# Kernel tuning notes

Hardware: AMD Instinct MI355X
Metric: run time of the kernel (lower is better)

Reference implementation:

```python
import jax, jax.numpy as jnp
import numpy as np

B, N = 32, 512
IN, HID, HEADS, OUT = 128, 32, 4, 128
NEG_SLOPE = 0.2


def _ln(x, g, b, eps=1e-5):
    mu = x.mean(-1, keepdims=True)
    var = ((x - mu) ** 2).mean(-1, keepdims=True)
    return (x - mu) * jax.lax.rsqrt(var + eps) * g + b


def _gat(x, adj_mask, W, a_src, a_dst, average):
    # x: [B,N,F], adj_mask: [B,1,N,N] bool, W: [F,H,D], a_*: [H,D]
    h = jnp.einsum('bnf,fhd->bnhd', x, W)                      # [B,N,H,D]
    e_src = jnp.einsum('bnhd,hd->bhn', h, a_src)               # [B,H,N]
    e_dst = jnp.einsum('bnhd,hd->bhn', h, a_dst)
    e = jax.nn.leaky_relu(e_src[:, :, :, None] + e_dst[:, :, None, :], NEG_SLOPE)  # [B,H,N,N]
    e = jnp.where(adj_mask, e, jnp.asarray(-1e9, e.dtype))
    att = jax.nn.softmax(e, axis=-1)                           # masked softmax over neighbors
    out = jnp.einsum('bhnm,bmhd->bnhd', att, h)                # aggregate neighbor features
    if average:
        return out.mean(axis=2)                                # [B,N,D]
    return out.reshape(out.shape[0], out.shape[1], -1)         # concat heads [B,N,H*D]


def setup_inputs() -> dict:
    key = jax.random.key(0)
    ks = jax.random.split(key, 16)
    def nrm(k, shape, scale=0.05):
        return jax.random.normal(k, shape, dtype=jnp.float32) * scale
    return {
        'x': jax.random.normal(ks[0], (B, N, IN), dtype=jnp.float32),
        'graph': jax.random.randint(ks[1], (B, N, N), 0, 2, dtype=jnp.int32),
        'W0': nrm(ks[2], (IN, HEADS, HID)),
        'a_src0': nrm(ks[3], (HEADS, HID)),
        'a_dst0': nrm(ks[4], (HEADS, HID)),
        'W1': nrm(ks[5], (HEADS * HID, 1, OUT)),
        'a_src1': nrm(ks[6], (1, OUT)),
        'a_dst1': nrm(ks[7], (1, OUT)),
        'ln1_g': jnp.ones((IN + OUT,), jnp.float32), 'ln1_b': jnp.zeros((IN + OUT,), jnp.float32),
        'lin_W': nrm(ks[8], (IN + OUT, OUT)), 'lin_b': jnp.zeros((OUT,), jnp.float32),
        'me_W0': nrm(ks[9], (OUT, OUT)), 'me_b0': jnp.zeros((OUT,), jnp.float32),
        'me_W1': nrm(ks[10], (OUT, OUT)), 'me_b1': jnp.zeros((OUT,), jnp.float32),
        'ln2_g': jnp.ones((OUT,), jnp.float32), 'ln2_b': jnp.zeros((OUT,), jnp.float32),
        'oh_W': nrm(ks[11], (OUT, OUT)), 'oh_b': jnp.zeros((OUT,), jnp.float32),
        'ln3_g': jnp.ones((OUT,), jnp.float32), 'ln3_b': jnp.zeros((OUT,), jnp.float32),
    }


def reference(x, graph, W0, a_src0, a_dst0, W1, a_src1, a_dst1,
              ln1_g, ln1_b, lin_W, lin_b, me_W0, me_b0, me_W1, me_b1,
              ln2_g, ln2_b, oh_W, oh_b, ln3_g, ln3_b):
    eye = jnp.eye(N, dtype=bool)
    adj_mask = ((graph > 0) | eye)[:, None, :, :]              # self-loops, [B,1,N,N]
    m = _gat(x, adj_mask, W0, a_src0, a_dst0, average=False)   # [B,N,HEADS*HID]
    m = jax.nn.elu(m)
    m = _gat(m, adj_mask, W1, a_src1, a_dst1, average=True)    # [B,N,OUT]
    m = _ln(jnp.concatenate([x, m], axis=-1), ln1_g, ln1_b)    # ln1
    m = m @ lin_W + lin_b                                      # linear
    enc = jax.nn.gelu(m @ me_W0 + me_b0, approximate=False) @ me_W1 + me_b1
    out = _ln(m + enc, ln2_g, ln2_b)                           # ln2(residual)
    out = jax.nn.gelu(out @ oh_W + oh_b, approximate=False)
    out = _ln(out, ln3_g, ln3_b)                               # LN inside output_head
    return out
```

## Files before the change

### kernel.cpp

```cpp
#include <hip/hip_runtime.h>
#include <cmath>


typedef unsigned short ushort_t;
typedef __attribute__((ext_vector_type(8))) short short8;
typedef __attribute__((ext_vector_type(4))) float f32x4;

__device__ __forceinline__ float gelu_f(float v) {
    return 0.5f * v * (1.0f + erff(v * 0.70710678118654752f));
}
__device__ __forceinline__ ushort_t f2bf(float x) {
    union { float f; unsigned u; } v; v.f = x;
    return (ushort_t)((v.u + 0x7FFFu + ((v.u >> 16) & 1u)) >> 16);
}
__device__ __forceinline__ ushort_t f2bf_t(float x) {
    union { float f; unsigned u; } v; v.f = x;
    return (ushort_t)(v.u >> 16);
}

__global__ __launch_bounds__(256) void prep_wt(const float* __restrict__ lin_W,
        const float* __restrict__ me_W0, const float* __restrict__ me_W1,
        const float* __restrict__ oh_W, const float* __restrict__ W0,
        const float* __restrict__ W1, ushort_t* __restrict__ WT) {
    int i = blockIdx.x * 256 + threadIdx.x;
    if (i < 32768)       { int c = i >> 8, k = i & 255;                   WT[i] = f2bf(lin_W[k * 128 + c]); }
    else if (i < 49152)  { int j = i - 32768;  int c = j >> 7, k = j & 127; WT[i] = f2bf(me_W0[k * 128 + c]); }
    else if (i < 65536)  { int j = i - 49152;  int c = j >> 7, k = j & 127; WT[i] = f2bf(me_W1[k * 128 + c]); }
    else if (i < 81920)  { int j = i - 65536;  int c = j >> 7, k = j & 127; WT[i] = f2bf(oh_W[k * 128 + c]); }
    else if (i < 98304)  { int j = i - 81920;  int c = j >> 7, k = j & 127; WT[i] = f2bf(W0[k * 128 + c]); }
    else if (i < 114688) { int j = i - 98304;  int c = j >> 7, k = j & 127; WT[i] = f2bf(W1[k * 128 + c]); }
}

template<int MODE>
__global__ __launch_bounds__(256) void gemm_mfma(const float* __restrict__ X,
        const ushort_t* __restrict__ WTr, ushort_t* __restrict__ Ht,
        const float* __restrict__ a_s, const float* __restrict__ a_d,
        float* __restrict__ es, float* __restrict__ ed) {
    __shared__ __align__(16) ushort_t abuf[16 * 128];
    __shared__ __align__(16) ushort_t tb[128 * 24];
    __shared__ float2 ered[8 * 16];
    const int tid = threadIdx.x;
    const int row0 = blockIdx.x * 16;
    const int b = row0 >> 9, m0 = row0 & 511;
    const int w = tid >> 6, lane = tid & 63;
    const int quad = lane >> 4, lid = lane & 15;
    {
        int r = tid >> 4, g = tid & 15;
        const float4* src = (const float4*)(X + (row0 + r) * 128 + g * 8);
        float4 a = src[0], bb = src[1];
        short8 p;
        p[0] = (short)f2bf(a.x);  p[1] = (short)f2bf(a.y);
        p[2] = (short)f2bf(a.z);  p[3] = (short)f2bf(a.w);
        p[4] = (short)f2bf(bb.x); p[5] = (short)f2bf(bb.y);
        p[6] = (short)f2bf(bb.z); p[7] = (short)f2bf(bb.w);
        *(short8*)&abuf[r * 128 + ((g ^ (r & 7)) * 8)] = p;
    }
    __syncthreads();
    short8 af[4];
#pragma unroll
    for (int kc = 0; kc < 4; kc++)
        af[kc] = *(const short8*)&abuf[lid * 128 + (((kc * 4 + quad) ^ (lid & 7)) * 8)];
    f32x4 C[2];
#pragma unroll
    for (int i = 0; i < 2; i++) {
        int ct = w + 4 * i;
        const ushort_t* bp = WTr + (ct * 16 + lid) * 128 + quad * 8;
        C[i] = (f32x4){0.f, 0.f, 0.f, 0.f};
#pragma unroll
        for (int kc = 0; kc < 4; kc++) {
            short8 bf = *(const short8*)&bp[kc * 32];
            C[i] = __builtin_amdgcn_mfma_f32_16x16x32_bf16(af[kc], bf, C[i], 0, 0, 0);
        }
    }
#pragma unroll
    for (int i = 0; i < 2; i++) {
        int ct = w + 4 * i, col = ct * 16 + lid;
        float as_c = a_s[col], ad_c = a_d[col];
        float s0[4], d0[4];
#pragma unroll
        for (int r = 0; r < 4; r++) { s0[r] = C[i][r] * as_c; d0[r] = C[i][r] * ad_c; }
#pragma unroll
        for (int st = 1; st <= 8; st <<= 1)
#pragma unroll
            for (int r = 0; r < 4; r++) {
                s0[r] += __shfl_xor(s0[r], st);
                d0[r] += __shfl_xor(d0[r], st);
            }
        if (lid == 0) {
#pragma unroll
            for (int r = 0; r < 4; r++)
                ered[ct * 16 + quad * 4 + r] = make_float2(s0[r], d0[r]);
        }
    }
#pragma unroll
    for (int i = 0; i < 2; i++) {
        int c = (w + 4 * i) * 16 + lid;
#pragma unroll
        for (int r = 0; r < 4; r++)
            tb[c * 24 + quad * 4 + r] = f2bf(C[i][r]);
    }
    __syncthreads();
    if (MODE == 0) {
        if (tid < 64) {
            int row = tid & 15, h = tid >> 4;
            float2 pa = ered[(2 * h) * 16 + row], pb = ered[(2 * h + 1) * 16 + row];
            es[(b * 4 + h) * 512 + m0 + row] = pa.x + pb.x;
            ed[(b * 4 + h) * 512 + m0 + row] = pa.y + pb.y;
        }
    } else {
        if (tid < 16) {
            float S = 0.f, D = 0.f;
#pragma unroll
            for (int ct = 0; ct < 8; ct++) { float2 p = ered[ct * 16 + tid]; S += p.x; D += p.y; }
            es[b * 512 + m0 + tid] = S;
            ed[b * 512 + m0 + tid] = D;
        }
    }
    {
        int c = tid >> 1, half = tid & 1;
        *(short8*)&Ht[b * 65536 + c * 512 + m0 + half * 8] = *(const short8*)&tb[c * 24 + half * 8];
    }
}

__global__ __launch_bounds__(256) void gat0_mfma(const ushort_t* __restrict__ Ht,
        const float* __restrict__ es0, const float* __restrict__ ed0,
        const int* __restrict__ graph, float* __restrict__ O) {
    __shared__ __align__(16) ushort_t hsb[128 * 64];
    __shared__ __align__(16) ushort_t ps[64 * 64];
    __shared__ float eds[2048];
    __shared__ float ess[64];
    const int tid = threadIdx.x;
    const int b = blockIdx.y, n0 = blockIdx.x * 16;
    const int lane = tid & 63, wv = tid >> 6;
    const int quad = lane >> 4, lid = lane & 15;
    const int pn = tid >> 4, pg = (tid >> 1) & 7, ph = tid & 1;
    for (int i = tid; i < 2048; i += 256) eds[i] = ed0[b * 2048 + i];
    if (tid < 64) ess[tid] = es0[b * 2048 + (tid >> 4) * 512 + n0 + (tid & 15)];
    const short8 onesf = {0x3F80, 0x3F80, 0x3F80, 0x3F80, 0x3F80, 0x3F80, 0x3F80, 0x3F80};
    f32x4 acc[2], dsf;
    acc[0] = (f32x4){0.f, 0.f, 0.f, 0.f};
    acc[1] = (f32x4){0.f, 0.f, 0.f, 0.f};
    dsf = (f32x4){0.f, 0.f, 0.f, 0.f};
    for (int mc = 0; mc < 512; mc += 64) {
        __syncthreads();
        {
            const ushort_t* src = Ht + b * 65536 + mc;
            for (int u = tid; u < 1024; u += 256) {
                int c = u >> 3, g = u & 7;
                *(short8*)&hsb[c * 64 + ((g ^ (c & 7)) * 8)] = *(const short8*)&src[c * 512 + g * 8];
            }
        }
        {
            int ng = n0 + pn, mbase = mc + pg * 8;
            const int* grow = graph + (b * 512 + ng) * 512 + mbase;
            int4 ga = *(const int4*)grow;
            int4 gb = *(const int4*)(grow + 4);
            int gv[8] = {ga.x, ga.y, ga.z, ga.w, gb.x, gb.y, gb.z, gb.w};
            bool keep[8];
#pragma unroll
            for (int j = 0; j < 8; j++)
                keep[j] = (gv[j] > 0) | ((mbase + j) == ng);
#pragma unroll
            for (int hi = 0; hi < 2; hi++) {
                int hh = ph * 2 + hi;
                float es_v = ess[hh * 16 + pn];
                float4 e0v = *(const float4*)&eds[hh * 512 + mbase];
                float4 e1v = *(const float4*)&eds[hh * 512 + mbase + 4];
                float ev[8] = {e0v.x, e0v.y, e0v.z, e0v.w, e1v.x, e1v.y, e1v.z, e1v.w};
                short8 pk;
#pragma unroll
                for (int j = 0; j < 8; j++) {
                    float e = es_v + ev[j];
                    e = fmaxf(e, 0.2f * e);
                    e = keep[j] ? e : -1e30f;
                    pk[j] = (short)f2bf_t(__expf(e));
                }
                int prow = hh * 16 + pn;
                *(short8*)&ps[prow * 64 + ((pg ^ (prow & 7)) * 8)] = pk;
            }
        }
        __syncthreads();
#pragma unroll
        for (int kc = 0; kc < 2; kc++) {
            const int gsw = ((kc * 4 + quad) ^ (lid & 7)) * 8;
            short8 a = *(const short8*)&ps[(wv * 16 + lid) * 64 + gsw];
            short8 b0f = *(const short8*)&hsb[(wv * 32 + lid) * 64 + gsw];
            short8 b1f = *(const short8*)&hsb[(wv * 32 + 16 + lid) * 64 + gsw];
            acc[0] = __builtin_amdgcn_mfma_f32_16x16x32_bf16(a, b0f, acc[0], 0, 0, 0);
            acc[1] = __builtin_amdgcn_mfma_f32_16x16x32_bf16(a, b1f, acc[1], 0, 0, 0);
            dsf = __builtin_amdgcn_mfma_f32_16x16x32_bf16(a, onesf, dsf, 0, 0, 0);
        }
    }
#pragma unroll
    for (int reg = 0; reg < 4; reg++) {
        float inv = 1.0f / dsf[reg];
        int row = b * 512 + n0 + quad * 4 + reg;
#pragma unroll
        for (int ch = 0; ch < 2; ch++) {
            float v = acc[ch][reg] * inv;
            v = v > 0.f ? v : expm1f(v);
            O[row * 128 + wv * 32 + ch * 16 + lid] = v;
        }
    }
}

__global__ __launch_bounds__(256) void gat1_mfma(const ushort_t* __restrict__ Ht,
        const float* __restrict__ es1, const float* __restrict__ ed1,
        const int* __restrict__ graph, float* __restrict__ O) {
    __shared__ __align__(16) ushort_t hsb[128 * 64];
    __shared__ __align__(16) ushort_t ps[16 * 64];
    __shared__ float eds[512];
    __shared__ float ess[16];
    const int tid = threadIdx.x;
    const int b = blockIdx.y, n0 = blockIdx.x * 16;
    const int lane = tid & 63, wv = tid >> 6;
    const int quad = lane >> 4, lid = lane & 15;
    for (int i = tid; i < 512; i += 256) eds[i] = ed1[b * 512 + i];
    if (tid < 16) ess[tid] = es1[b * 512 + n0 + tid];
    const short8 onesf = {0x3F80, 0x3F80, 0x3F80, 0x3F80, 0x3F80, 0x3F80, 0x3F80, 0x3F80};
    f32x4 acc[2], dsf;
    acc[0] = (f32x4){0.f, 0.f, 0.f, 0.f};
    acc[1] = (f32x4){0.f, 0.f, 0.f, 0.f};
    dsf = (f32x4){0.f, 0.f, 0.f, 0.f};
    for (int mc = 0; mc < 512; mc += 64) {
        __syncthreads();
        {
            const ushort_t* src = Ht + b * 65536 + mc;
            for (int u = tid; u < 1024; u += 256) {
                int c = u >> 3, g = u & 7;
                *(short8*)&hsb[c * 64 + ((g ^ (c & 7)) * 8)] = *(const short8*)&src[c * 512 + g * 8];
            }
        }
        if (tid < 128) {
            int pn = tid >> 3, pg = tid & 7;
            int ng = n0 + pn, mbase = mc + pg * 8;
            const int* grow = graph + (b * 512 + ng) * 512 + mbase;
            int4 ga = *(const int4*)grow;
            int4 gb = *(const int4*)(grow + 4);
            int gv[8] = {ga.x, ga.y, ga.z, ga.w, gb.x, gb.y, gb.z, gb.w};
            float4 e0v = *(const float4*)&eds[mbase & 511];
            float4 e1v = *(const float4*)&eds[(mbase & 511) + 4];
            float ev[8] = {e0v.x, e0v.y, e0v.z, e0v.w, e1v.x, e1v.y, e1v.z, e1v.w};
            float es_v = ess[pn];
            short8 pk;
#pragma unroll
            for (int j = 0; j < 8; j++) {
                float e = es_v + ev[j];
                e = fmaxf(e, 0.2f * e);
                e = ((gv[j] > 0) | ((mbase + j) == ng)) ? e : -1e30f;
                pk[j] = (short)f2bf_t(__expf(e));
            }
            *(short8*)&ps[pn * 64 + ((pg ^ (pn & 7)) * 8)] = pk;
        }
        __syncthreads();
#pragma unroll
        for (int kc = 0; kc < 2; kc++) {
            const int gsw = ((kc * 4 + quad) ^ (lid & 7)) * 8;
            short8 a = *(const short8*)&ps[lid * 64 + gsw];
            short8 b0f = *(const short8*)&hsb[(wv * 32 + lid) * 64 + gsw];
            short8 b1f = *(const short8*)&hsb[(wv * 32 + 16 + lid) * 64 + gsw];
            acc[0] = __builtin_amdgcn_mfma_f32_16x16x32_bf16(a, b0f, acc[0], 0, 0, 0);
            acc[1] = __builtin_amdgcn_mfma_f32_16x16x32_bf16(a, b1f, acc[1], 0, 0, 0);
            dsf = __builtin_amdgcn_mfma_f32_16x16x32_bf16(a, onesf, dsf, 0, 0, 0);
        }
    }
#pragma unroll
    for (int reg = 0; reg < 4; reg++) {
        float inv = 1.0f / dsf[reg];
        int row = b * 512 + n0 + quad * 4 + reg;
#pragma unroll
        for (int ch = 0; ch < 2; ch++)
            O[row * 128 + wv * 32 + ch * 16 + lid] = acc[ch][reg] * inv;
    }
}

__global__ __launch_bounds__(256) void head_fused(const float* __restrict__ x,
        const float* __restrict__ G, const float* __restrict__ g1, const float* __restrict__ b1,
        const ushort_t* __restrict__ linT, const float* __restrict__ LB,
        const ushort_t* __restrict__ meT0, const float* __restrict__ B0,
        const ushort_t* __restrict__ meT1, const float* __restrict__ B1,
        const float* __restrict__ g2, const float* __restrict__ b2,
        const ushort_t* __restrict__ ohT, const float* __restrict__ ob,
        const float* __restrict__ g3, const float* __restrict__ b3,
        float* __restrict__ out) {
    __shared__ __align__(16) ushort_t ybuf[16 * 256];
    __shared__ __align__(16) ushort_t abuf[16 * 128];
    __shared__ __align__(16) ushort_t tbuf[16 * 128];
    __shared__ float2 red[4 * 16];
    __shared__ float2 mvs[16];
    const int tid = threadIdx.x;
    const int row0 = blockIdx.x * 16;
    const int w = tid >> 6, lane = tid & 63;
    const int quad = lane >> 4, lid = lane & 15;
    const int r = tid >> 4, c16 = tid & 15;
    const float4* xp = (const float4*)(x + (row0 + r) * 128);
    const float4* gp = (const float4*)(G + (row0 + r) * 128);
    float4 vv4[4];
    float s = 0.f, ss = 0.f;
#pragma unroll
    for (int i = 0; i < 4; i++) {
        int c4 = c16 * 4 + i;
        float4 v = (c4 < 32) ? xp[c4] : gp[c4 - 32];
        vv4[i] = v;
        s += v.x + v.y + v.z + v.w;
        ss += v.x * v.x + v.y * v.y + v.z * v.z + v.w * v.w;
    }
#pragma unroll
    for (int st = 1; st <= 8; st <<= 1) { s += __shfl_xor(s, st); ss += __shfl_xor(ss, st); }
    if (c16 == 0) {
        float mu = s * (1.f / 256.f);
        float var = ss * (1.f / 256.f) - mu * mu;
        mvs[r] = make_float2(mu, rsqrtf(var + 1e-5f));
    }
    __syncthreads();
    {
        float mu = mvs[r].x, rstd = mvs[r].y;
#pragma unroll
        for (int half = 0; half < 2; half++) {
            int g = c16 * 2 + half, c0 = g * 8;
            float va[8] = {vv4[half * 2].x, vv4[half * 2].y, vv4[half * 2].z, vv4[half * 2].w,
                           vv4[half * 2 + 1].x, vv4[half * 2 + 1].y, vv4[half * 2 + 1].z, vv4[half * 2 + 1].w};
            short8 p;
#pragma unroll
            for (int e = 0; e < 8; e++)
                p[e] = (short)f2bf((va[e] - mu) * rstd * g1[c0 + e] + b1[c0 + e]);
            *(short8*)&ybuf[r * 256 + ((g ^ (r & 7)) * 8)] = p;
        }
    }
    __syncthreads();
    short8 af8[8];
#pragma unroll
    for (int ks = 0; ks < 8; ks++)
        af8[ks] = *(const short8*)&ybuf[lid * 256 + (((ks * 4 + quad) ^ (lid & 7)) * 8)];
    f32x4 M2[2];
#pragma unroll
    for (int i = 0; i < 2; i++) {
        int ct = w + 4 * i;
        const ushort_t* bp = linT + (ct * 16 + lid) * 256 + quad * 8;
        M2[i] = (f32x4){0.f, 0.f, 0.f, 0.f};
#pragma unroll
        for (int ks = 0; ks < 8; ks++) {
            short8 bf = *(const short8*)&bp[ks * 32];
            M2[i] = __builtin_amdgcn_mfma_f32_16x16x32_bf16(af8[ks], bf, M2[i], 0, 0, 0);
        }
        float bias = LB[ct * 16 + lid];
#pragma unroll
        for (int reg = 0; reg < 4; reg++) M2[i][reg] += bias;
        int col = ct * 16 + lid, g = col >> 3, pos = col & 7;
#pragma unroll
        for (int reg = 0; reg < 4; reg++) {
            int rw = quad * 4 + reg;
            abuf[rw * 128 + ((g ^ (rw & 7)) * 8) + pos] = f2bf(M2[i][reg]);
        }
    }
    __syncthreads();
    short8 at[4];
#pragma unroll
    for (int kc = 0; kc < 4; kc++)
        at[kc] = *(const short8*)&abuf[lid * 128 + (((kc * 4 + quad) ^ (lid & 7)) * 8)];
#pragma unroll
    for (int i = 0; i < 2; i++) {
        int ct = w + 4 * i;
        const ushort_t* bp = meT0 + (ct * 16 + lid) * 128 + quad * 8;
        f32x4 C = (f32x4){0.f, 0.f, 0.f, 0.f};
#pragma unroll
        for (int kc = 0; kc < 4; kc++) {
            short8 bf = *(const short8*)&bp[kc * 32];
            C = __builtin_amdgcn_mfma_f32_16x16x32_bf16(at[kc], bf, C, 0, 0, 0);
        }
        int col = ct * 16 + lid, g = col >> 3, pos = col & 7;
        float bias = B0[col];
#pragma unroll
        for (int reg = 0; reg < 4; reg++) {
            int rw = quad * 4 + reg;
            tbuf[rw * 128 + ((g ^ (rw & 7)) * 8) + pos] = f2bf(gelu_f(C[reg] + bias));
        }
    }
    __syncthreads();
#pragma unroll
    for (int kc = 0; kc < 4; kc++)
        at[kc] = *(const short8*)&tbuf[lid * 128 + (((kc * 4 + quad) ^ (lid & 7)) * 8)];
    f32x4 R[2];
    float sr[4] = {0.f, 0.f, 0.f, 0.f}, ssr[4] = {0.f, 0.f, 0.f, 0.f};
#pragma unroll
    for (int i = 0; i < 2; i++) {
        int ct = w + 4 * i;
        const ushort_t* bp = meT1 + (ct * 16 + lid) * 128 + quad * 8;
        f32x4 C = (f32x4){0.f, 0.f, 0.f, 0.f};
#pragma unroll
        for (int kc = 0; kc < 4; kc++) {
            short8 bf = *(const short8*)&bp[kc * 32];
            C = __builtin_amdgcn_mfma_f32_16x16x32_bf16(at[kc], bf, C, 0, 0, 0);
        }
        float bias = B1[ct * 16 + lid];
#pragma unroll
        for (int reg = 0; reg < 4; reg++) {
            float v = M2[i][reg] + C[reg] + bias;
            R[i][reg] = v;
            sr[reg] += v; ssr[reg] += v * v;
        }
    }
#pragma unroll
    for (int st = 1; st <= 8; st <<= 1)
#pragma unroll
        for (int reg = 0; reg < 4; reg++) {
            sr[reg] += __shfl_xor(sr[reg], st);
            ssr[reg] += __shfl_xor(ssr[reg], st);
        }
    if (lid == 0) {
#pragma unroll
        for (int reg = 0; reg < 4; reg++)
            red[w * 16 + quad * 4 + reg] = make_float2(sr[reg], ssr[reg]);
    }
    __syncthreads();
    float mu2[4], rstd2[4];
#pragma unroll
    for (int reg = 0; reg < 4; reg++) {
        float S = 0.f, SS = 0.f;
#pragma unroll
        for (int w4 = 0; w4 < 4; w4++) {
            float2 p = red[w4 * 16 + quad * 4 + reg];
            S += p.x; SS += p.y;
        }
        mu2[reg] = S * (1.f / 128.f);
        float var = SS * (1.f / 128.f) - mu2[reg] * mu2[reg];
        rstd2[reg] = rsqrtf(var + 1e-5f);
    }
#pragma unroll
    for (int i = 0; i < 2; i++) {
        int col = (w + 4 * i) * 16 + lid, g = col >> 3, pos = col & 7;
        float gv = g2[col], bv = b2[col];
#pragma unroll
        for (int reg = 0; reg < 4; reg++) {
            int rw = quad * 4 + reg;
            float v = (R[i][reg] - mu2[reg]) * rstd2[reg] * gv + bv;
            tbuf[rw * 128 + ((g ^ (rw & 7)) * 8) + pos] = f2bf(v);
        }
    }
    __syncthreads();
#pragma unroll
    for (int kc = 0; kc < 4; kc++)
        at[kc] = *(const short8*)&tbuf[lid * 128 + (((kc * 4 + quad) ^ (lid & 7)) * 8)];
    f32x4 V[2];
#pragma unroll
    for (int reg = 0; reg < 4; reg++) { sr[reg] = 0.f; ssr[reg] = 0.f; }
#pragma unroll
    for (int i = 0; i < 2; i++) {
        int ct = w + 4 * i;
        const ushort_t* bp = ohT + (ct * 16 + lid) * 128 + quad * 8;
        f32x4 C = (f32x4){0.f, 0.f, 0.f, 0.f};
#pragma unroll
        for (int kc = 0; kc < 4; kc++) {
            short8 bf = *(const short8*)&bp[kc * 32];
            C = __builtin_amdgcn_mfma_f32_16x16x32_bf16(at[kc], bf, C, 0, 0, 0);
        }
        float bias = ob[ct * 16 + lid];
#pragma unroll
        for (int reg = 0; reg < 4; reg++) {
            float v = gelu_f(C[reg] + bias);
            V[i][reg] = v;
            sr[reg] += v; ssr[reg] += v * v;
        }
    }
#pragma unroll
    for (int st = 1; st <= 8; st <<= 1)
#pragma unroll
        for (int reg = 0; reg < 4; reg++) {
            sr[reg] += __shfl_xor(sr[reg], st);
            ssr[reg] += __shfl_xor(ssr[reg], st);
        }
    if (lid == 0) {
#pragma unroll
        for (int reg = 0; reg < 4; reg++)
            red[w * 16 + quad * 4 + reg] = make_float2(sr[reg], ssr[reg]);
    }
    __syncthreads();
#pragma unroll
    for (int reg = 0; reg < 4; reg++) {
        float S = 0.f, SS = 0.f;
#pragma unroll
        for (int w4 = 0; w4 < 4; w4++) {
            float2 p = red[w4 * 16 + quad * 4 + reg];
            S += p.x; SS += p.y;
        }
        mu2[reg] = S * (1.f / 128.f);
        float var = SS * (1.f / 128.f) - mu2[reg] * mu2[reg];
        rstd2[reg] = rsqrtf(var + 1e-5f);
    }
#pragma unroll
    for (int i = 0; i < 2; i++) {
        int col = (w + 4 * i) * 16 + lid;
        float gv = g3[col], bv = b3[col];
#pragma unroll
        for (int reg = 0; reg < 4; reg++)
            out[(row0 + quad * 4 + reg) * 128 + col] =
                (V[i][reg] - mu2[reg]) * rstd2[reg] * gv + bv;
    }
}

extern "C" void kernel_launch(void* const* d_in, const int* in_sizes, int n_in,
                              void* d_out, int out_size, void* d_ws, size_t ws_size,
                              hipStream_t stream) {
    const float* x      = (const float*)d_in[0];
    const int*   graph  = (const int*)d_in[1];
    const float* a_src0 = (const float*)d_in[3];
    const float* a_dst0 = (const float*)d_in[4];
    const float* a_src1 = (const float*)d_in[6];
    const float* a_dst1 = (const float*)d_in[7];
    const float* ln1_g  = (const float*)d_in[8];
    const float* ln1_b  = (const float*)d_in[9];
    const float* lin_b  = (const float*)d_in[11];
    const float* me_b0  = (const float*)d_in[13];
    const float* me_b1  = (const float*)d_in[15];
    const float* ln2_g  = (const float*)d_in[16];
    const float* ln2_b  = (const float*)d_in[17];
    const float* oh_b   = (const float*)d_in[19];
    const float* ln3_g  = (const float*)d_in[20];
    const float* ln3_b  = (const float*)d_in[21];
    float* out = (float*)d_out;

    float* ws  = (float*)d_ws;
    float*    fA   = ws;
    float*    fB   = ws + 2097152;
    ushort_t* Ht   = (ushort_t*)(ws + 4194304);
    float*    e0s  = ws + 5242880;
    float*    e0d  = e0s + 65536;
    float*    e1s  = e0d + 65536;
    float*    e1d  = e1s + 16384;
    ushort_t* WT   = (ushort_t*)(e1d + 16384);
    ushort_t* linT = WT;
    ushort_t* meT0 = WT + 32768;
    ushort_t* meT1 = WT + 49152;
    ushort_t* ohT  = WT + 65536;
    ushort_t* W0T  = WT + 81920;
    ushort_t* W1T  = WT + 98304;

    prep_wt<<<448, 256, 0, stream>>>((const float*)d_in[10], (const float*)d_in[12],
                                     (const float*)d_in[14], (const float*)d_in[18],
                                     (const float*)d_in[2], (const float*)d_in[5], WT);
    gemm_mfma<0><<<1024, 256, 0, stream>>>(x, W0T, Ht, a_src0, a_dst0, e0s, e0d);
    gat0_mfma<<<dim3(32, 32), 256, 0, stream>>>(Ht, e0s, e0d, graph, fB);
    gemm_mfma<1><<<1024, 256, 0, stream>>>(fB, W1T, Ht, a_src1, a_dst1, e1s, e1d);
    gat1_mfma<<<dim3(32, 32), 256, 0, stream>>>(Ht, e1s, e1d, graph, fA);
    head_fused<<<1024, 256, 0, stream>>>(x, fA, ln1_g, ln1_b, linT, lin_b,
                                         meT0, me_b0, meT1, me_b1, ln2_g, ln2_b,
                                         ohT, oh_b, ln3_g, ln3_b, out);
}
```

Before: 205.4 us.

## Fuse layer-1 projection into GAT0 and head into GAT1 kernels

Merges the second projection GEMM into the epilogue of the first GAT aggregation kernel, and merges the LN/MLP head into the epilogue of the second GAT kernel. Kernel launches drop from six to four. The fp32 intermediate activations no longer make a round trip through global memory and are passed through aliased shared memory instead. Shared memory is reused with extra barriers, and the heavier kernels may lower occupancy.

Measured after the change: 198.5 us. 3.3% less time.

```diff
diff --git a/kernel.cpp b/kernel.cpp
--- a/kernel.cpp
+++ b/kernel.cpp
@@ -31,8 +31,7 @@
     else if (i < 114688) { int j = i - 98304;  int c = j >> 7, k = j & 127; WT[i] = f2bf(W1[k * 128 + c]); }
 }
 
-template<int MODE>
-__global__ __launch_bounds__(256) void gemm_mfma(const float* __restrict__ X,
+__global__ __launch_bounds__(256) void gemm_mfma0(const float* __restrict__ X,
         const ushort_t* __restrict__ WTr, ushort_t* __restrict__ Ht,
         const float* __restrict__ a_s, const float* __restrict__ a_d,
         float* __restrict__ es, float* __restrict__ ed) {
@@ -91,30 +90,16 @@
             for (int r = 0; r < 4; r++)
                 ered[ct * 16 + quad * 4 + r] = make_float2(s0[r], d0[r]);
         }
-    }
-#pragma unroll
-    for (int i = 0; i < 2; i++) {
-        int c = (w + 4 * i) * 16 + lid;
 #pragma unroll
         for (int r = 0; r < 4; r++)
-            tb[c * 24 + quad * 4 + r] = f2bf(C[i][r]);
-    }
-    __syncthreads();
-    if (MODE == 0) {
-        if (tid < 64) {
-            int row = tid & 15, h = tid >> 4;
-            float2 pa = ered[(2 * h) * 16 + row], pb = ered[(2 * h + 1) * 16 + row];
-            es[(b * 4 + h) * 512 + m0 + row] = pa.x + pb.x;
-            ed[(b * 4 + h) * 512 + m0 + row] = pa.y + pb.y;
-        }
-    } else {
-        if (tid < 16) {
-            float S = 0.f, D = 0.f;
-#pragma unroll
-            for (int ct = 0; ct < 8; ct++) { float2 p = ered[ct * 16 + tid]; S += p.x; D += p.y; }
-            es[b * 512 + m0 + tid] = S;
-            ed[b * 512 + m0 + tid] = D;
-        }
+            tb[col * 24 + quad * 4 + r] = f2bf(C[i][r]);
+    }
+    __syncthreads();
+    if (tid < 64) {
+        int row = tid & 15, h = tid >> 4;
+        float2 pa = ered[(2 * h) * 16 + row], pb = ered[(2 * h + 1) * 16 + row];
+        es[(b * 4 + h) * 512 + m0 + row] = pa.x + pb.x;
+        ed[(b * 4 + h) * 512 + m0 + row] = pa.y + pb.y;
     }
     {
         int c = tid >> 1, half = tid & 1;
@@ -122,13 +107,19 @@
     }
 }
 
-__global__ __launch_bounds__(256) void gat0_mfma(const ushort_t* __restrict__ Ht,
+__global__ __launch_bounds__(256) void gat0_gemm(const ushort_t* __restrict__ Ht0,
         const float* __restrict__ es0, const float* __restrict__ ed0,
-        const int* __restrict__ graph, float* __restrict__ O) {
-    __shared__ __align__(16) ushort_t hsb[128 * 64];
-    __shared__ __align__(16) ushort_t ps[64 * 64];
-    __shared__ float eds[2048];
-    __shared__ float ess[64];
+        const int* __restrict__ graph, const ushort_t* __restrict__ W1T,
+        const float* __restrict__ a_s, const float* __restrict__ a_d,
+        ushort_t* __restrict__ Ht1, float* __restrict__ es1, float* __restrict__ ed1) {
+    __shared__ __align__(16) char smem[33024];
+    ushort_t* hsb  = (ushort_t*)smem;
+    ushort_t* ps   = (ushort_t*)(smem + 16384);
+    float*    eds  = (float*)(smem + 24576);
+    float*    ess  = (float*)(smem + 32768);
+    ushort_t* abuf = (ushort_t*)(smem + 16384);
+    ushort_t* tb   = (ushort_t*)(smem + 24576);
+    float2*   ered = (float2*)(smem + 30720);
     const int tid = threadIdx.x;
     const int b = blockIdx.y, n0 = blockIdx.x * 16;
     const int lane = tid & 63, wv = tid >> 6;
@@ -144,7 +135,7 @@
     for (int mc = 0; mc < 512; mc += 64) {
         __syncthreads();
         {
-            const ushort_t* src = Ht + b * 65536 + mc;
+            const ushort_t* src = Ht0 + b * 65536 + mc;
             for (int u = tid; u < 1024; u += 256) {
                 int c = u >> 3, g = u & 7;
                 *(short8*)&hsb[c * 64 + ((g ^ (c & 7)) * 8)] = *(const short8*)&src[c * 512 + g * 8];
@@ -191,26 +182,95 @@
             dsf = __builtin_amdgcn_mfma_f32_16x16x32_bf16(a, onesf, dsf, 0, 0, 0);
         }
     }
+    __syncthreads();
 #pragma unroll
     for (int reg = 0; reg < 4; reg++) {
         float inv = 1.0f / dsf[reg];
-        int row = b * 512 + n0 + quad * 4 + reg;
+        int rw = quad * 4 + reg;
 #pragma unroll
         for (int ch = 0; ch < 2; ch++) {
             float v = acc[ch][reg] * inv;
             v = v > 0.f ? v : expm1f(v);
-            O[row * 128 + wv * 32 + ch * 16 + lid] = v;
-        }
-    }
-}
-
-__global__ __launch_bounds__(256) void gat1_mfma(const ushort_t* __restrict__ Ht,
+            int col = wv * 32 + ch * 16 + lid;
+            abuf[rw * 128 + (((col >> 3) ^ (rw & 7)) * 8) + (col & 7)] = f2bf(v);
+        }
+    }
+    __syncthreads();
+    short8 af[4];
+#pragma unroll
+    for (int kc = 0; kc < 4; kc++)
+        af[kc] = *(const short8*)&abuf[lid * 128 + (((kc * 4 + quad) ^ (lid & 7)) * 8)];
+    f32x4 C[2];
+#pragma unroll
+    for (int i = 0; i < 2; i++) {
+        int ct = wv + 4 * i;
+        const ushort_t* bp = W1T + (ct * 16 + lid) * 128 + quad * 8;
+        C[i] = (f32x4){0.f, 0.f, 0.f, 0.f};
+#pragma unroll
+        for (int kc = 0; kc < 4; kc++) {
+            short8 bf = *(const short8*)&bp[kc * 32];
+            C[i] = __builtin_amdgcn_mfma_f32_16x16x32_bf16(af[kc], bf, C[i], 0, 0, 0);
+        }
+    }
+#pragma unroll
+    for (int i = 0; i < 2; i++) {
+        int ct = wv + 4 * i, col = ct * 16 + lid;
+        float as_c = a_s[col], ad_c = a_d[col];
+        float s0[4], d0[4];
+#pragma unroll
+        for (int r = 0; r < 4; r++) { s0[r] = C[i][r] * as_c; d0[r] = C[i][r] * ad_c; }
+#pragma unroll
+        for (int st = 1; st <= 8; st <<= 1)
+#pragma unroll
+            for (int r = 0; r < 4; r++) {
+                s0[r] += __shfl_xor(s0[r], st);
+                d0[r] += __shfl_xor(d0[r], st);
+            }
+        if (lid == 0) {
+#pragma unroll
+            for (int r = 0; r < 4; r++)
+                ered[ct * 16 + quad * 4 + r] = make_float2(s0[r], d0[r]);
+        }
+#pragma unroll
+        for (int r = 0; r < 4; r++)
+            tb[col * 24 + quad * 4 + r] = f2bf(C[i][r]);
+    }
+    __syncthreads();
+    if (tid < 16) {
+        float S = 0.f, D = 0.f;
+#pragma unroll
+        for (int ct = 0; ct < 8; ct++) { float2 p = ered[ct * 16 + tid]; S += p.x; D += p.y; }
+        es1[b * 512 + n0 + tid] = S;
+        ed1[b * 512 + n0 + tid] = D;
+    }
+    {
+        int c = tid >> 1, half = tid & 1;
+        *(short8*)&Ht1[b * 65536 + c * 512 + n0 + half * 8] = *(const short8*)&tb[c * 24 + half * 8];
+    }
+}
+
+__global__ __launch_bounds__(256) void gat1_head(const ushort_t* __restrict__ Ht,
         const float* __restrict__ es1, const float* __restrict__ ed1,
-        const int* __restrict__ graph, float* __restrict__ O) {
-    __shared__ __align__(16) ushort_t hsb[128 * 64];
-    __shared__ __align__(16) ushort_t ps[16 * 64];
-    __shared__ float eds[512];
-    __shared__ float ess[16];
+        const int* __restrict__ graph, const float* __restrict__ x,
+        const float* __restrict__ g1, const float* __restrict__ b1,
+        const ushort_t* __restrict__ linT, const float* __restrict__ LB,
+        const ushort_t* __restrict__ meT0, const float* __restrict__ B0,
+        const ushort_t* __restrict__ meT1, const float* __restrict__ B1,
+        const float* __restrict__ g2, const float* __restrict__ b2,
+        const ushort_t* __restrict__ ohT, const float* __restrict__ ob,
+        const float* __restrict__ g3, const float* __restrict__ b3,
+        float* __restrict__ out) {
+    __shared__ __align__(16) char smem[25472];
+    ushort_t* hsb  = (ushort_t*)smem;
+    ushort_t* ps   = (ushort_t*)(smem + 16384);
+    float*    eds  = (float*)(smem + 18432);
+    float*    ess  = (float*)(smem + 20480);
+    ushort_t* ybuf = (ushort_t*)smem;
+    ushort_t* abuf = (ushort_t*)(smem + 8192);
+    ushort_t* tbuf = (ushort_t*)(smem + 12288);
+    float*    gbuf = (float*)(smem + 16384);
+    float2*   red  = (float2*)(smem + 24832);
+    float2*   mvs  = (float2*)(smem + 25344);
     const int tid = threadIdx.x;
     const int b = blockIdx.y, n0 = blockIdx.x * 16;
     const int lane = tid & 63, wv = tid >> 6;
@@ -264,43 +324,24 @@
             dsf = __builtin_amdgcn_mfma_f32_16x16x32_bf16(a, onesf, dsf, 0, 0, 0);
         }
     }
+    __syncthreads();
 #pragma unroll
     for (int reg = 0; reg < 4; reg++) {
         float inv = 1.0f / dsf[reg];
-        int row = b * 512 + n0 + quad * 4 + reg;
+        int rw = quad * 4 + reg;
 #pragma unroll
         for (int ch = 0; ch < 2; ch++)
-            O[row * 128 + wv * 32 + ch * 16 + lid] = acc[ch][reg] * inv;
-    }
-}
-
-__global__ __launch_bounds__(256) void head_fused(const float* __restrict__ x,
-        const float* __restrict__ G, const float* __restrict__ g1, const float* __restrict__ b1,
-        const ushort_t* __restrict__ linT, const float* __restrict__ LB,
-        const ushort_t* __restrict__ meT0, const float* __restrict__ B0,
-        const ushort_t* __restrict__ meT1, const float* __restrict__ B1,
-        const float* __restrict__ g2, const float* __restrict__ b2,
-        const ushort_t* __restrict__ ohT, const float* __restrict__ ob,
-        const float* __restrict__ g3, const float* __restrict__ b3,
-        float* __restrict__ out) {
-    __shared__ __align__(16) ushort_t ybuf[16 * 256];
-    __shared__ __align__(16) ushort_t abuf[16 * 128];
-    __shared__ __align__(16) ushort_t tbuf[16 * 128];
-    __shared__ float2 red[4 * 16];
-    __shared__ float2 mvs[16];
-    const int tid = threadIdx.x;
-    const int row0 = blockIdx.x * 16;
-    const int w = tid >> 6, lane = tid & 63;
-    const int quad = lane >> 4, lid = lane & 15;
+            gbuf[rw * 132 + wv * 32 + ch * 16 + lid] = acc[ch][reg] * inv;
+    }
+    __syncthreads();
     const int r = tid >> 4, c16 = tid & 15;
-    const float4* xp = (const float4*)(x + (row0 + r) * 128);
-    const float4* gp = (const float4*)(G + (row0 + r) * 128);
+    const float4* xp = (const float4*)(x + (b * 512 + n0 + r) * 128);
     float4 vv4[4];
     float s = 0.f, ss = 0.f;
 #pragma unroll
     for (int i = 0; i < 4; i++) {
         int c4 = c16 * 4 + i;
-        float4 v = (c4 < 32) ? xp[c4] : gp[c4 - 32];
+        float4 v = (c4 < 32) ? xp[c4] : *(const float4*)&gbuf[r * 132 + (c4 - 32) * 4];
         vv4[i] = v;
         s += v.x + v.y + v.z + v.w;
         ss += v.x * v.x + v.y * v.y + v.z * v.z + v.w * v.w;
@@ -335,7 +376,7 @@
     f32x4 M2[2];
 #pragma unroll
     for (int i = 0; i < 2; i++) {
-        int ct = w + 4 * i;
+        int ct = wv + 4 * i;
         const ushort_t* bp = linT + (ct * 16 + lid) * 256 + quad * 8;
         M2[i] = (f32x4){0.f, 0.f, 0.f, 0.f};
 #pragma unroll
@@ -360,7 +401,7 @@
         at[kc] = *(const short8*)&abuf[lid * 128 + (((kc * 4 + quad) ^ (lid & 7)) * 8)];
 #pragma unroll
     for (int i = 0; i < 2; i++) {
-        int ct = w + 4 * i;
+        int ct = wv + 4 * i;
         const ushort_t* bp = meT0 + (ct * 16 + lid) * 128 + quad * 8;
         f32x4 C = (f32x4){0.f, 0.f, 0.f, 0.f};
 #pragma unroll
@@ -384,7 +425,7 @@
     float sr[4] = {0.f, 0.f, 0.f, 0.f}, ssr[4] = {0.f, 0.f, 0.f, 0.f};
 #pragma unroll
     for (int i = 0; i < 2; i++) {
-        int ct = w + 4 * i;
+        int ct = wv + 4 * i;
         const ushort_t* bp = meT1 + (ct * 16 + lid) * 128 + quad * 8;
         f32x4 C = (f32x4){0.f, 0.f, 0.f, 0.f};
 #pragma unroll
@@ -410,7 +451,7 @@
     if (lid == 0) {
 #pragma unroll
         for (int reg = 0; reg < 4; reg++)
-            red[w * 16 + quad * 4 + reg] = make_float2(sr[reg], ssr[reg]);
+            red[wv * 16 + quad * 4 + reg] = make_float2(sr[reg], ssr[reg]);
     }
     __syncthreads();
     float mu2[4], rstd2[4];
@@ -428,7 +469,7 @@
     }
 #pragma unroll
     for (int i = 0; i < 2; i++) {
-        int col = (w + 4 * i) * 16 + lid, g = col >> 3, pos = col & 7;
+        int col = (wv + 4 * i) * 16 + lid, g = col >> 3, pos = col & 7;
         float gv = g2[col], bv = b2[col];
 #pragma unroll
         for (int reg = 0; reg < 4; reg++) {
@@ -446,7 +487,7 @@
     for (int reg = 0; reg < 4; reg++) { sr[reg] = 0.f; ssr[reg] = 0.f; }
 #pragma unroll
     for (int i = 0; i < 2; i++) {
-        int ct = w + 4 * i;
+        int ct = wv + 4 * i;
         const ushort_t* bp = ohT + (ct * 16 + lid) * 128 + quad * 8;
         f32x4 C = (f32x4){0.f, 0.f, 0.f, 0.f};
 #pragma unroll
@@ -472,7 +513,7 @@
     if (lid == 0) {
 #pragma unroll
         for (int reg = 0; reg < 4; reg++)
-            red[w * 16 + quad * 4 + reg] = make_float2(sr[reg], ssr[reg]);
+            red[wv * 16 + quad * 4 + reg] = make_float2(sr[reg], ssr[reg]);
     }
     __syncthreads();
 #pragma unroll
@@ -489,11 +530,11 @@
     }
 #pragma unroll
     for (int i = 0; i < 2; i++) {
-        int col = (w + 4 * i) * 16 + lid;
+        int col = (wv + 4 * i) * 16 + lid;
         float gv = g3[col], bv = b3[col];
 #pragma unroll
         for (int reg = 0; reg < 4; reg++)
-            out[(row0 + quad * 4 + reg) * 128 + col] =
+            out[(b * 512 + n0 + quad * 4 + reg) * 128 + col] =
                 (V[i][reg] - mu2[reg]) * rstd2[reg] * gv + bv;
     }
 }
@@ -507,23 +548,12 @@
     const float* a_dst0 = (const float*)d_in[4];
     const float* a_src1 = (const float*)d_in[6];
     const float* a_dst1 = (const float*)d_in[7];
-    const float* ln1_g  = (const float*)d_in[8];
-    const float* ln1_b  = (const float*)d_in[9];
-    const float* lin_b  = (const float*)d_in[11];
-    const float* me_b0  = (const float*)d_in[13];
-    const float* me_b1  = (const float*)d_in[15];
-    const float* ln2_g  = (const float*)d_in[16];
-    const float* ln2_b  = (const float*)d_in[17];
-    const float* oh_b   = (const float*)d_in[19];
-    const float* ln3_g  = (const float*)d_in[20];
-    const float* ln3_b  = (const float*)d_in[21];
     float* out = (float*)d_out;
 
     float* ws  = (float*)d_ws;
-    float*    fA   = ws;
-    float*    fB   = ws + 2097152;
-    ushort_t* Ht   = (ushort_t*)(ws + 4194304);
-    float*    e0s  = ws + 5242880;
+    ushort_t* Ht0  = (ushort_t*)ws;
+    ushort_t* Ht1  = Ht0 + 2097152;
+    float*    e0s  = ws + 2097152;
     float*    e0d  = e0s + 65536;
     float*    e1s  = e0d + 65536;
     float*    e1d  = e1s + 16384;
@@ -538,11 +568,16 @@
     prep_wt<<<448, 256, 0, stream>>>((const float*)d_in[10], (const float*)d_in[12],
                                      (const float*)d_in[14], (const float*)d_in[18],
                                      (const float*)d_in[2], (const float*)d_in[5], WT);
-    gemm_mfma<0><<<1024, 256, 0, stream>>>(x, W0T, Ht, a_src0, a_dst0, e0s, e0d);
-    gat0_mfma<<<dim3(32, 32), 256, 0, stream>>>(Ht, e0s, e0d, graph, fB);
-    gemm_mfma<1><<<1024, 256, 0, stream>>>(fB, W1T, Ht, a_src1, a_dst1, e1s, e1d);
-    gat1_mfma<<<dim3(32, 32), 256, 0, stream>>>(Ht, e1s, e1d, graph, fA);
-    head_fused<<<1024, 256, 0, stream>>>(x, fA, ln1_g, ln1_b, linT, lin_b,
-                                         meT0, me_b0, meT1, me_b1, ln2_g, ln2_b,
-                                         ohT, oh_b, ln3_g, ln3_b, out);
-}
+    gemm_mfma0<<<1024, 256, 0, stream>>>(x, W0T, Ht0, a_src0, a_dst0, e0s, e0d);
+    gat0_gemm<<<dim3(32, 32), 256, 0, stream>>>(Ht0, e0s, e0d, graph, W1T,
+                                                a_src1, a_dst1, Ht1, e1s, e1d);
+    gat1_head<<<dim3(32, 32), 256, 0, stream>>>(Ht1, e1s, e1d, graph, x,
+                                                (const float*)d_in[8], (const float*)d_in[9],
+                                                linT, (const float*)d_in[11],
+                                                meT0, (const float*)d_in[13],
+                                                meT1, (const float*)d_in[15],
+                                                (const float*)d_in[16], (const float*)d_in[17],
+                                                ohT, (const float*)d_in[19],
+                                                (const float*)d_in[20], (const float*)d_in[21],
+                                                out);
+}
```
